# Kernel tuning notes

Measured on AMD Instinct MI355X. Metric: run time of the kernel, lower is better.

The kernel has to match this reference:

```python
import jax, jax.numpy as jnp
import numpy as np

NUM_HEADS = 12
QK_SCALE = 1.0
EPS = 1e-12  # torch.nn.functional.normalize default eps


def _l2norm(t):
    # matches torch F.normalize: x / max(||x||_2, eps) along last axis
    n = jnp.sqrt(jnp.sum(t * t, axis=-1, keepdims=True))
    return t / jnp.maximum(n, EPS)


def setup_inputs() -> dict:
    key = jax.random.key(0)
    k1, k2 = jax.random.split(key)
    B, N, dim = 8, 4096, 768
    x = jax.random.normal(k1, (B, N, 3 * dim), dtype=jnp.float32)
    temperature = jnp.ones((NUM_HEADS, 1, 1), dtype=jnp.float32)
    proj_w = jax.random.normal(k2, (dim, dim), dtype=jnp.float32) * (1.0 / np.sqrt(dim))
    proj_b = jnp.zeros((dim,), dtype=jnp.float32)
    return {"x": x, "temperature": temperature, "proj_w": proj_w, "proj_b": proj_b}


def reference(x, temperature, proj_w, proj_b):
    B, N, C3 = x.shape
    C = C3 // 3
    H = NUM_HEADS
    d = C // H
    # (B, N, 3, H, d) -> (3, B, H, N, d)
    qkv = x.reshape(B, N, 3, H, d).transpose(2, 0, 3, 1, 4)
    q, k, v = qkv[0], qkv[1], qkv[2]
    q = jnp.swapaxes(q, -2, -1) * QK_SCALE   # [B, H, d, N]
    v = jnp.swapaxes(v, -2, -1)              # [B, H, d, N]
    q = _l2norm(q)                           # normalize over tokens N
    k = _l2norm(k)                           # normalize over head dim d (k is [B,H,N,d])
    # cross-covariance attention over channels: [B, H, d, d]
    attn = jnp.einsum('bhdn,bhne->bhde', q, k) * temperature
    attn = jax.nn.softmax(attn, axis=-1)
    out = jnp.einsum('bhde,bhen->bhdn', attn, v)  # [B, H, d, N]
    out = out.transpose(0, 3, 1, 2).reshape(B, N, C)  # [B, N, C]
    out = out @ proj_w.T + proj_b
    return out
```

## Files before the change

kernel.cpp:

```cpp
#include <hip/hip_runtime.h>
#include <hip/hip_bf16.h>

#define BB 8
#define NN 4096
#define HH 12
#define CC 768
#define C3 2304

typedef float  f32x4  __attribute__((ext_vector_type(4)));
typedef __bf16 bf16x8 __attribute__((ext_vector_type(8)));
typedef __bf16 bf16x4 __attribute__((ext_vector_type(4)));

__device__ __forceinline__ void gload16(const void* g, void* l) {
  __builtin_amdgcn_global_load_lds((const __attribute__((address_space(1))) void*)g,
                                   (__attribute__((address_space(3))) void*)l, 16, 0, 0);
}

__global__ __launch_bounds__(256) void k0_vcvt(const float* __restrict__ x,
                                               __bf16* __restrict__ vb) {
  const int idx = blockIdx.x * 256 + threadIdx.x;
  const int bn = idx / 192;
  const int c4 = (idx - bn * 192) * 4;
  const float4 v = *(const float4*)(x + (size_t)bn * C3 + 1536 + c4);
  bf16x4 r;
  r[0] = (__bf16)v.x; r[1] = (__bf16)v.y; r[2] = (__bf16)v.z; r[3] = (__bf16)v.w;
  *(bf16x4*)(vb + (size_t)bn * CC + c4) = r;
}

__global__ __launch_bounds__(256) void k1_logits(const float* __restrict__ x,
                                                 float* __restrict__ S,
                                                 float* __restrict__ qss) {
  const int slice = blockIdx.x, h = blockIdx.y, b = blockIdx.z;
  const int tid = threadIdx.x;
  __shared__ float qb[8][68];
  __shared__ float kb[8][68];
  __shared__ float invk[8];

  const int t8     = tid >> 5;
  const int lane32 = tid & 31;
  const bool isQ   = lane32 < 16;
  const int col4   = (lane32 & 15) * 4;
  const int i0     = tid >> 4;
  const int jc     = tid & 15;

  float acc[4][4];
#pragma unroll
  for (int r = 0; r < 4; ++r)
#pragma unroll
    for (int c = 0; c < 4; ++c) acc[r][c] = 0.f;
  float qsl[4] = {0.f, 0.f, 0.f, 0.f};

  for (int g = 0; g < 32; ++g) {
    const int n = slice * 256 + g * 8 + t8;
    const float* p = x + (size_t)(b * NN + n) * C3 + (isQ ? 0 : 768) + h * 64 + col4;
    const float4 v = *(const float4*)p;
    __syncthreads();
    if (isQ) *(float4*)&qb[t8][col4] = v;
    else     *(float4*)&kb[t8][col4] = v;
    __syncthreads();
    {
      const float a = kb[t8][lane32];
      const float c = kb[t8][lane32 + 32];
      float ps = a * a + c * c;
      ps += __shfl_xor(ps, 1);
      ps += __shfl_xor(ps, 2);
      ps += __shfl_xor(ps, 4);
      ps += __shfl_xor(ps, 8);
      ps += __shfl_xor(ps, 16);
      if (lane32 == 0) invk[t8] = 1.0f / fmaxf(sqrtf(ps), 1e-12f);
    }
    __syncthreads();
#pragma unroll
    for (int t = 0; t < 8; ++t) {
      const float inv = invk[t];
      float4 kv = *(const float4*)&kb[t][jc * 4];
      kv.x *= inv; kv.y *= inv; kv.z *= inv; kv.w *= inv;
#pragma unroll
      for (int r = 0; r < 4; ++r) {
        const float qv = qb[t][i0 + 16 * r];
        acc[r][0] = fmaf(qv, kv.x, acc[r][0]);
        acc[r][1] = fmaf(qv, kv.y, acc[r][1]);
        acc[r][2] = fmaf(qv, kv.z, acc[r][2]);
        acc[r][3] = fmaf(qv, kv.w, acc[r][3]);
        if (jc == 0) qsl[r] = fmaf(qv, qv, qsl[r]);
      }
    }
  }

  float* Sp = S + (size_t)(b * HH + h) * 4096;
#pragma unroll
  for (int r = 0; r < 4; ++r) {
    const int i = i0 + 16 * r;
#pragma unroll
    for (int c = 0; c < 4; ++c)
      atomicAdd(&Sp[i * 64 + jc * 4 + c], acc[r][c]);
    if (jc == 0) atomicAdd(&qss[(b * HH + h) * 64 + i], qsl[r]);
  }
}

__global__ __launch_bounds__(64) void k2_softmax(const float* __restrict__ S,
                                                 const float* __restrict__ qss,
                                                 const float* __restrict__ temp,
                                                 float* __restrict__ attn) {
  const int h = blockIdx.x, b = blockIdx.y;
  const int i = threadIdx.x;
  const size_t bh = (size_t)(b * HH + h);
  const float rqs = 1.0f / fmaxf(sqrtf(qss[bh * 64 + i]), 1e-12f);
  const float tp  = temp[h] * rqs;
  const float* Sp = S + bh * 4096 + i * 64;
  float v[64];
  float m = -3.4e38f;
#pragma unroll
  for (int j = 0; j < 64; ++j) { v[j] = Sp[j] * tp; m = fmaxf(m, v[j]); }
  float s = 0.f;
#pragma unroll
  for (int j = 0; j < 64; ++j) { v[j] = __expf(v[j] - m); s += v[j]; }
  const float inv = 1.0f / s;
  float* Ap = attn + bh * 4096 + i * 64;
#pragma unroll
  for (int j = 0; j < 64; ++j) Ap[j] = v[j] * inv;
}

__global__ __launch_bounds__(256) void k3_w2(const float* __restrict__ attn,
                                             const float* __restrict__ pw,
                                             __bf16* __restrict__ W2) {
  const int ct = blockIdx.x, h = blockIdx.y, b = blockIdx.z;
  const int co0 = ct * 64;
  __shared__ float pT[64][65];
  __shared__ float ab[64][64];
  const int tid = threadIdx.x;
  const int r = tid >> 2, c0 = (tid & 3) * 16;
  {
    const float* pp = pw + (size_t)(co0 + r) * CC + h * 64 + c0;
    const float4 p0 = *(const float4*)(pp + 0);
    const float4 p1 = *(const float4*)(pp + 4);
    const float4 p2 = *(const float4*)(pp + 8);
    const float4 p3 = *(const float4*)(pp + 12);
    const float* ap = attn + (size_t)(b * HH + h) * 4096 + r * 64 + c0;
    const float4 a0 = *(const float4*)(ap + 0);
    const float4 a1 = *(const float4*)(ap + 4);
    const float4 a2 = *(const float4*)(ap + 8);
    const float4 a3 = *(const float4*)(ap + 12);
    pT[c0 +  0][r] = p0.x; pT[c0 +  1][r] = p0.y; pT[c0 +  2][r] = p0.z; pT[c0 +  3][r] = p0.w;
    pT[c0 +  4][r] = p1.x; pT[c0 +  5][r] = p1.y; pT[c0 +  6][r] = p1.z; pT[c0 +  7][r] = p1.w;
    pT[c0 +  8][r] = p2.x; pT[c0 +  9][r] = p2.y; pT[c0 + 10][r] = p2.z; pT[c0 + 11][r] = p2.w;
    pT[c0 + 12][r] = p3.x; pT[c0 + 13][r] = p3.y; pT[c0 + 14][r] = p3.z; pT[c0 + 15][r] = p3.w;
    *(float4*)&ab[r][c0 + 0]  = a0;
    *(float4*)&ab[r][c0 + 4]  = a1;
    *(float4*)&ab[r][c0 + 8]  = a2;
    *(float4*)&ab[r][c0 + 12] = a3;
  }
  __syncthreads();
  const int col = tid & 63, jg = tid >> 6;
  float accJ[16];
#pragma unroll
  for (int c = 0; c < 16; ++c) accJ[c] = 0.f;
#pragma unroll 4
  for (int i = 0; i < 64; ++i) {
    const float p = pT[i][col];
    const float4* a4 = (const float4*)&ab[i][jg * 16];
    const float4 A0 = a4[0], A1 = a4[1], A2 = a4[2], A3 = a4[3];
    accJ[0]  = fmaf(p, A0.x, accJ[0]);  accJ[1]  = fmaf(p, A0.y, accJ[1]);
    accJ[2]  = fmaf(p, A0.z, accJ[2]);  accJ[3]  = fmaf(p, A0.w, accJ[3]);
    accJ[4]  = fmaf(p, A1.x, accJ[4]);  accJ[5]  = fmaf(p, A1.y, accJ[5]);
    accJ[6]  = fmaf(p, A1.z, accJ[6]);  accJ[7]  = fmaf(p, A1.w, accJ[7]);
    accJ[8]  = fmaf(p, A2.x, accJ[8]);  accJ[9]  = fmaf(p, A2.y, accJ[9]);
    accJ[10] = fmaf(p, A2.z, accJ[10]); accJ[11] = fmaf(p, A2.w, accJ[11]);
    accJ[12] = fmaf(p, A3.x, accJ[12]); accJ[13] = fmaf(p, A3.y, accJ[13]);
    accJ[14] = fmaf(p, A3.z, accJ[14]); accJ[15] = fmaf(p, A3.w, accJ[15]);
  }
  bf16x8 u0, u1;
#pragma unroll
  for (int c = 0; c < 8; ++c) { u0[c] = (__bf16)accJ[c]; u1[c] = (__bf16)accJ[8 + c]; }
  __bf16* wp = W2 + ((size_t)b * CC + co0 + col) * CC + h * 64 + jg * 16;
  *(bf16x8*)(wp)     = u0;
  *(bf16x8*)(wp + 8) = u1;
}

__global__ __launch_bounds__(256) void k4_gemm(const __bf16* __restrict__ vb,
                                               const __bf16* __restrict__ W2,
                                               const float* __restrict__ pb,
                                               float* __restrict__ out) {
  int id = blockIdx.x;
  const int bz = id / 192;
  const int rem = id - bz * 192;
  const int mg = rem / 48;
  const int idx = rem - mg * 48;
  const int nt = idx >> 3;
  const int mt = mg * 8 + (idx & 7);
  const int m0 = mt * 128, co0 = nt * 128;

  __shared__ __bf16 At[128][32];
  __shared__ __bf16 Bt[128][32];

  const int tid  = threadIdx.x;
  const int w    = tid >> 6, lane = tid & 63;
  const int wm   = w >> 1,   wn   = w & 1;
  const int fr   = lane & 15;
  const int fk   = lane >> 4;

  f32x4 acc[4][4];
#pragma unroll
  for (int tm = 0; tm < 4; ++tm)
#pragma unroll
    for (int tn = 0; tn < 4; ++tn) acc[tm][tn] = (f32x4){0.f, 0.f, 0.f, 0.f};

  const int srow = lane >> 2;
  const int scol = (lane & 3) * 8;
  const __bf16* Ag = vb + (size_t)(bz * NN + m0 + w * 32 + srow) * CC + scol;
  const __bf16* Bg = W2 + ((size_t)bz * CC + co0 + w * 32 + srow) * CC + scol;
  __bf16* lA0 = &At[w * 32][0];
  __bf16* lA1 = &At[w * 32 + 16][0];
  __bf16* lB0 = &Bt[w * 32][0];
  __bf16* lB1 = &Bt[w * 32 + 16][0];

  for (int kk = 0; kk < 24; ++kk) {
    const int kb = kk * 32;
    __syncthreads();
    gload16(Ag + kb,            lA0);
    gload16(Ag + 16 * CC + kb,  lA1);
    gload16(Bg + kb,            lB0);
    gload16(Bg + 16 * CC + kb,  lB1);
    __syncthreads();
    bf16x8 afr[4], bfr[4];
#pragma unroll
    for (int tm = 0; tm < 4; ++tm)
      afr[tm] = *(const bf16x8*)&At[wm * 64 + tm * 16 + fr][fk * 8];
#pragma unroll
    for (int tn = 0; tn < 4; ++tn)
      bfr[tn] = *(const bf16x8*)&Bt[wn * 64 + tn * 16 + fr][fk * 8];
#pragma unroll
    for (int tm = 0; tm < 4; ++tm)
#pragma unroll
      for (int tn = 0; tn < 4; ++tn)
        acc[tm][tn] = __builtin_amdgcn_mfma_f32_16x16x32_bf16(afr[tm], bfr[tn],
                                                              acc[tm][tn], 0, 0, 0);
  }

#pragma unroll
  for (int tn = 0; tn < 4; ++tn) {
    const int co = co0 + wn * 64 + tn * 16 + fr;
    const float bias = pb[co];
#pragma unroll
    for (int tm = 0; tm < 4; ++tm) {
#pragma unroll
      for (int rr = 0; rr < 4; ++rr) {
        const int row = m0 + wm * 64 + tm * 16 + fk * 4 + rr;
        out[(size_t)(bz * NN + row) * CC + co] = acc[tm][tn][rr] + bias;
      }
    }
  }
}

extern "C" void kernel_launch(void* const* d_in, const int* in_sizes, int n_in,
                              void* d_out, int out_size, void* d_ws, size_t ws_size,
                              hipStream_t stream) {
  const float* x    = (const float*)d_in[0];
  const float* temp = (const float*)d_in[1];
  const float* pw   = (const float*)d_in[2];
  const float* pb   = (const float*)d_in[3];
  float* out = (float*)d_out;
  char* ws = (char*)d_ws;

  float*  S    = (float*)(ws);
  float*  qss  = (float*)(ws + 1572864);
  float*  attn = (float*)(ws + 1597440);
  __bf16* W2   = (__bf16*)(ws + 3170304);
  __bf16* vb   = (__bf16*)(ws + 12607488);

  hipMemsetAsync(ws, 0, 1597440, stream);

  hipLaunchKernelGGL(k0_vcvt,    dim3(24576),     dim3(256), 0, stream, x, vb);
  hipLaunchKernelGGL(k1_logits,  dim3(16, 12, 8), dim3(256), 0, stream, x, S, qss);
  hipLaunchKernelGGL(k2_softmax, dim3(12, 8),     dim3(64),  0, stream, S, qss, temp, attn);
  hipLaunchKernelGGL(k3_w2,      dim3(12, 12, 8), dim3(256), 0, stream, attn, pw, W2);
  hipLaunchKernelGGL(k4_gemm,    dim3(1536),      dim3(256), 0, stream, vb, W2, pb, out);
}
```

Measured before the change: 615.5 us.

## Compute q·k logits with bf16 MFMA and deterministic partial-sum reduction

The q·k cross-covariance kernel now stages transposed bf16 q and normalized k tiles in shared memory and uses 16x16x32 bf16 MFMA instead of scalar FMAs. Each block covers 512 tokens instead of 256. Partial logits and q-square sums go to per-slice buffers that the softmax kernel reduces, which removes the atomics and the workspace memset. This trades fp32 precision in the logits for bf16 inputs and adds extra partial-buffer traffic in the softmax kernel.

```diff
diff --git a/kernel.cpp b/kernel.cpp
--- a/kernel.cpp
+++ b/kernel.cpp
@@ -28,95 +28,118 @@
 }
 
 __global__ __launch_bounds__(256) void k1_logits(const float* __restrict__ x,
-                                                 float* __restrict__ S,
-                                                 float* __restrict__ qss) {
-  const int slice = blockIdx.x, h = blockIdx.y, b = blockIdx.z;
+                                                 float* __restrict__ Spart,
+                                                 float* __restrict__ Qpart) {
+  const int slice = blockIdx.x;
+  const int h = blockIdx.y, b = blockIdx.z;
   const int tid = threadIdx.x;
-  __shared__ float qb[8][68];
-  __shared__ float kb[8][68];
-  __shared__ float invk[8];
-
-  const int t8     = tid >> 5;
-  const int lane32 = tid & 31;
-  const bool isQ   = lane32 < 16;
-  const int col4   = (lane32 & 15) * 4;
-  const int i0     = tid >> 4;
-  const int jc     = tid & 15;
-
-  float acc[4][4];
-#pragma unroll
-  for (int r = 0; r < 4; ++r)
-#pragma unroll
-    for (int c = 0; c < 4; ++c) acc[r][c] = 0.f;
-  float qsl[4] = {0.f, 0.f, 0.f, 0.f};
-
-  for (int g = 0; g < 32; ++g) {
-    const int n = slice * 256 + g * 8 + t8;
-    const float* p = x + (size_t)(b * NN + n) * C3 + (isQ ? 0 : 768) + h * 64 + col4;
-    const float4 v = *(const float4*)p;
-    __syncthreads();
-    if (isQ) *(float4*)&qb[t8][col4] = v;
-    else     *(float4*)&kb[t8][col4] = v;
-    __syncthreads();
-    {
-      const float a = kb[t8][lane32];
-      const float c = kb[t8][lane32 + 32];
-      float ps = a * a + c * c;
-      ps += __shfl_xor(ps, 1);
-      ps += __shfl_xor(ps, 2);
-      ps += __shfl_xor(ps, 4);
-      ps += __shfl_xor(ps, 8);
-      ps += __shfl_xor(ps, 16);
-      if (lane32 == 0) invk[t8] = 1.0f / fmaxf(sqrtf(ps), 1e-12f);
+  __shared__ __bf16 qT[64][40];
+  __shared__ __bf16 kT[64][40];
+  __shared__ float  qws[4][64];
+
+  const int t   = tid >> 3;
+  const int sub = tid & 7;
+  const int w   = tid >> 6, lane = tid & 63;
+  const int fr  = lane & 15, fk = lane >> 4;
+
+  const float* qbase = x + (size_t)(b * NN + slice * 512) * C3 + h * 64 + sub * 8;
+
+  float qss8[8];
+#pragma unroll
+  for (int j = 0; j < 8; ++j) qss8[j] = 0.f;
+  f32x4 acc[4];
+#pragma unroll
+  for (int tn = 0; tn < 4; ++tn) acc[tn] = (f32x4){0.f, 0.f, 0.f, 0.f};
+
+  for (int step = 0; step < 16; ++step) {
+    const float* qp = qbase + (size_t)(step * 32 + t) * C3;
+    const float4 q0 = *(const float4*)(qp);
+    const float4 q1 = *(const float4*)(qp + 4);
+    const float4 k0 = *(const float4*)(qp + 768);
+    const float4 k1 = *(const float4*)(qp + 772);
+    float ss = k0.x * k0.x + k0.y * k0.y + k0.z * k0.z + k0.w * k0.w +
+               k1.x * k1.x + k1.y * k1.y + k1.z * k1.z + k1.w * k1.w;
+    ss += __shfl_xor(ss, 1);
+    ss += __shfl_xor(ss, 2);
+    ss += __shfl_xor(ss, 4);
+    const float inv = 1.0f / fmaxf(sqrtf(ss), 1e-12f);
+    __syncthreads();
+    const int c0 = sub * 8;
+    qT[c0 + 0][t] = (__bf16)q0.x; qT[c0 + 1][t] = (__bf16)q0.y;
+    qT[c0 + 2][t] = (__bf16)q0.z; qT[c0 + 3][t] = (__bf16)q0.w;
+    qT[c0 + 4][t] = (__bf16)q1.x; qT[c0 + 5][t] = (__bf16)q1.y;
+    qT[c0 + 6][t] = (__bf16)q1.z; qT[c0 + 7][t] = (__bf16)q1.w;
+    kT[c0 + 0][t] = (__bf16)(k0.x * inv); kT[c0 + 1][t] = (__bf16)(k0.y * inv);
+    kT[c0 + 2][t] = (__bf16)(k0.z * inv); kT[c0 + 3][t] = (__bf16)(k0.w * inv);
+    kT[c0 + 4][t] = (__bf16)(k1.x * inv); kT[c0 + 5][t] = (__bf16)(k1.y * inv);
+    kT[c0 + 6][t] = (__bf16)(k1.z * inv); kT[c0 + 7][t] = (__bf16)(k1.w * inv);
+    qss8[0] = fmaf(q0.x, q0.x, qss8[0]); qss8[1] = fmaf(q0.y, q0.y, qss8[1]);
+    qss8[2] = fmaf(q0.z, q0.z, qss8[2]); qss8[3] = fmaf(q0.w, q0.w, qss8[3]);
+    qss8[4] = fmaf(q1.x, q1.x, qss8[4]); qss8[5] = fmaf(q1.y, q1.y, qss8[5]);
+    qss8[6] = fmaf(q1.z, q1.z, qss8[6]); qss8[7] = fmaf(q1.w, q1.w, qss8[7]);
+    __syncthreads();
+    const bf16x8 afr = *(const bf16x8*)&qT[w * 16 + fr][fk * 8];
+#pragma unroll
+    for (int tn = 0; tn < 4; ++tn) {
+      const bf16x8 bfr = *(const bf16x8*)&kT[tn * 16 + fr][fk * 8];
+      acc[tn] = __builtin_amdgcn_mfma_f32_16x16x32_bf16(afr, bfr, acc[tn], 0, 0, 0);
     }
-    __syncthreads();
-#pragma unroll
-    for (int t = 0; t < 8; ++t) {
-      const float inv = invk[t];
-      float4 kv = *(const float4*)&kb[t][jc * 4];
-      kv.x *= inv; kv.y *= inv; kv.z *= inv; kv.w *= inv;
-#pragma unroll
-      for (int r = 0; r < 4; ++r) {
-        const float qv = qb[t][i0 + 16 * r];
-        acc[r][0] = fmaf(qv, kv.x, acc[r][0]);
-        acc[r][1] = fmaf(qv, kv.y, acc[r][1]);
-        acc[r][2] = fmaf(qv, kv.z, acc[r][2]);
-        acc[r][3] = fmaf(qv, kv.w, acc[r][3]);
-        if (jc == 0) qsl[r] = fmaf(qv, qv, qsl[r]);
-      }
-    }
-  }
-
-  float* Sp = S + (size_t)(b * HH + h) * 4096;
-#pragma unroll
-  for (int r = 0; r < 4; ++r) {
-    const int i = i0 + 16 * r;
-#pragma unroll
-    for (int c = 0; c < 4; ++c)
-      atomicAdd(&Sp[i * 64 + jc * 4 + c], acc[r][c]);
-    if (jc == 0) atomicAdd(&qss[(b * HH + h) * 64 + i], qsl[r]);
-  }
-}
-
-__global__ __launch_bounds__(64) void k2_softmax(const float* __restrict__ S,
-                                                 const float* __restrict__ qss,
+  }
+
+  const int bh = b * HH + h;
+  float* Sp = Spart + ((size_t)(slice * 96 + bh)) * 4096;
+#pragma unroll
+  for (int tn = 0; tn < 4; ++tn)
+#pragma unroll
+    for (int rr = 0; rr < 4; ++rr)
+      Sp[(w * 16 + fk * 4 + rr) * 64 + tn * 16 + fr] = acc[tn][rr];
+
+#pragma unroll
+  for (int j = 0; j < 8; ++j) {
+    float v = qss8[j];
+    v += __shfl_xor(v, 8);
+    v += __shfl_xor(v, 16);
+    v += __shfl_xor(v, 32);
+    if (lane < 8) qws[w][lane * 8 + j] = v;
+  }
+  __syncthreads();
+  if (tid < 64) {
+    const float qs = qws[0][tid] + qws[1][tid] + qws[2][tid] + qws[3][tid];
+    Qpart[((size_t)(slice * 96 + bh)) * 64 + tid] = qs;
+  }
+}
+
+__global__ __launch_bounds__(64) void k2_softmax(const float* __restrict__ Spart,
+                                                 const float* __restrict__ Qpart,
                                                  const float* __restrict__ temp,
                                                  float* __restrict__ attn) {
   const int h = blockIdx.x, b = blockIdx.y;
   const int i = threadIdx.x;
-  const size_t bh = (size_t)(b * HH + h);
-  const float rqs = 1.0f / fmaxf(sqrtf(qss[bh * 64 + i]), 1e-12f);
+  const int bh = b * HH + h;
+  float qs = 0.f;
+#pragma unroll
+  for (int s = 0; s < 8; ++s) qs += Qpart[((size_t)(s * 96 + bh)) * 64 + i];
+  float v[64];
+#pragma unroll
+  for (int j = 0; j < 64; ++j) v[j] = 0.f;
+  for (int s = 0; s < 8; ++s) {
+    const float* Sp = Spart + ((size_t)(s * 96 + bh)) * 4096 + i * 64;
+#pragma unroll
+    for (int j = 0; j < 64; j += 4) {
+      const float4 t4 = *(const float4*)(Sp + j);
+      v[j] += t4.x; v[j + 1] += t4.y; v[j + 2] += t4.z; v[j + 3] += t4.w;
+    }
+  }
+  const float rqs = 1.0f / fmaxf(sqrtf(qs), 1e-12f);
   const float tp  = temp[h] * rqs;
-  const float* Sp = S + bh * 4096 + i * 64;
-  float v[64];
   float m = -3.4e38f;
 #pragma unroll
-  for (int j = 0; j < 64; ++j) { v[j] = Sp[j] * tp; m = fmaxf(m, v[j]); }
+  for (int j = 0; j < 64; ++j) { v[j] *= tp; m = fmaxf(m, v[j]); }
   float s = 0.f;
 #pragma unroll
   for (int j = 0; j < 64; ++j) { v[j] = __expf(v[j] - m); s += v[j]; }
   const float inv = 1.0f / s;
-  float* Ap = attn + bh * 4096 + i * 64;
+  float* Ap = attn + (size_t)bh * 4096 + i * 64;
 #pragma unroll
   for (int j = 0; j < 64; ++j) Ap[j] = v[j] * inv;
 }
@@ -262,17 +285,15 @@
   float* out = (float*)d_out;
   char* ws = (char*)d_ws;
 
-  float*  S    = (float*)(ws);
-  float*  qss  = (float*)(ws + 1572864);
-  float*  attn = (float*)(ws + 1597440);
-  __bf16* W2   = (__bf16*)(ws + 3170304);
-  __bf16* vb   = (__bf16*)(ws + 12607488);
-
-  hipMemsetAsync(ws, 0, 1597440, stream);
-
-  hipLaunchKernelGGL(k0_vcvt,    dim3(24576),     dim3(256), 0, stream, x, vb);
-  hipLaunchKernelGGL(k1_logits,  dim3(16, 12, 8), dim3(256), 0, stream, x, S, qss);
-  hipLaunchKernelGGL(k2_softmax, dim3(12, 8),     dim3(64),  0, stream, S, qss, temp, attn);
+  float*  Spart = (float*)(ws);
+  float*  Qpart = (float*)(ws + 12582912);
+  float*  attn  = (float*)(ws + 12779520);
+  __bf16* W2    = (__bf16*)(ws + 14352384);
+  __bf16* vb    = (__bf16*)(ws + 23789568);
+
+  hipLaunchKernelGGL(k0_vcvt,    dim3(24576),    dim3(256), 0, stream, x, vb);
+  hipLaunchKernelGGL(k1_logits,  dim3(8, 12, 8), dim3(256), 0, stream, x, Spart, Qpart);
+  hipLaunchKernelGGL(k2_softmax, dim3(12, 8),    dim3(64),  0, stream, Spart, Qpart, temp, attn);
   hipLaunchKernelGGL(k3_w2,      dim3(12, 12, 8), dim3(256), 0, stream, attn, pw, W2);
-  hipLaunchKernelGGL(k4_gemm,    dim3(1536),      dim3(256), 0, stream, vb, W2, pb, out);
-}
+  hipLaunchKernelGGL(k4_gemm,    dim3(1536),     dim3(256), 0, stream, vb, W2, pb, out);
+}
```

After: 534.4 us. 1.15x faster.
